# Performance work log

Measured on AMD Instinct MI355X. Metric: run time of the kernel, lower is better.

Reference implementation:

```python
import jax, jax.numpy as jnp
import numpy as np

N_NODES = 10000
N_EDGES = 640000
IN_CH = 128
HID = 256
OUT_CH = 10
NUM_GRAPHS = 64
EPS = 0.0  # non-trainable buffer, initial_eps=0


def setup_inputs() -> dict:
    key = jax.random.key(0)
    ks = jax.random.split(key, 12)
    x = jax.random.normal(ks[0], (N_NODES, IN_CH), dtype=jnp.float32)
    edge_index = jax.random.randint(ks[1], (2, N_EDGES), 0, N_NODES, dtype=jnp.int64)
    batch = jnp.sort(jax.random.randint(ks[2], (N_NODES,), 0, NUM_GRAPHS, dtype=jnp.int64))
    edge_weights = jax.random.uniform(ks[3], (N_EDGES,), dtype=jnp.float32)
    def lin(k, fan_in, fan_out):
        bound = 1.0 / np.sqrt(fan_in)
        kw, kb = jax.random.split(k)
        W = jax.random.uniform(kw, (fan_out, fan_in), minval=-bound, maxval=bound, dtype=jnp.float32)
        b = jax.random.uniform(kb, (fan_out,), minval=-bound, maxval=bound, dtype=jnp.float32)
        return W, b
    W1, b1 = lin(ks[4], IN_CH, HID)
    W2, b2 = lin(ks[5], HID, HID)
    W3, b3 = lin(ks[6], HID, HID)
    Wl, bl = lin(ks[7], HID, OUT_CH)
    return {"x": x, "edge_index": edge_index, "batch": batch, "edge_weights": edge_weights,
            "W1": W1, "b1": b1, "W2": W2, "b2": b2, "W3": W3, "b3": b3, "Wl": Wl, "bl": bl}


def _ginw_conv(x, edge_index, edge_weights, W, b):
    # message: edge_weight * x_j (source nodes), aggregated by add at target i
    src, dst = edge_index[0], edge_index[1]
    msg = edge_weights[:, None] * x[src]           # [E, F]
    agg = jax.ops.segment_sum(msg, dst, num_segments=N_NODES)  # [N, F]
    out = agg + (1.0 + EPS) * x
    return out @ W.T + b


def reference(x, edge_index, batch, edge_weights, W1, b1, W2, b2, W3, b3, Wl, bl):
    h = jax.nn.relu(_ginw_conv(x, edge_index, edge_weights, W1, b1))
    h = jax.nn.relu(_ginw_conv(h, edge_index, edge_weights, W2, b2))
    h = jax.nn.relu(_ginw_conv(h, edge_index, edge_weights, W3, b3))
    # global mean pool over graphs
    sums = jax.ops.segment_sum(h, batch, num_segments=NUM_GRAPHS)        # [G, HID]
    cnts = jax.ops.segment_sum(jnp.ones((N_NODES,), h.dtype), batch, num_segments=NUM_GRAPHS)
    pooled = sums / jnp.maximum(cnts, 1.0)[:, None]
    return pooled @ Wl.T + bl
```

## Files before the change

### kernel.cpp

```cpp
#include <hip/hip_runtime.h>
#include <hip/hip_fp16.h>

namespace {
constexpr int NN   = 10000;
constexpr int NE   = 640000;
constexpr int INC  = 128;
constexpr int HIDC = 256;
constexpr int OUTC = 10;
constexpr int NG   = 64;
constexpr int PP   = 8;

constexpr int NB     = 157;
constexpr int G1     = 256;
constexpr int CHUNK1 = NE / G1;
constexpr int CAPB   = 64;
constexpr int LCAP   = 5120;
}

typedef __attribute__((ext_vector_type(8))) short short8;
typedef __attribute__((ext_vector_type(4))) float f32x4;

__device__ __forceinline__ ushort f2bf(float f) {
    uint u = __float_as_uint(f);
    uint r = u + 0x7FFFu + ((u >> 16) & 1u);
    return (ushort)(r >> 16);
}
__device__ __forceinline__ float bf2f(ushort u) {
    return __uint_as_float(((uint)u) << 16);
}
__device__ __forceinline__ float rec_w(uint rec) {
    return __half2float(__ushort_as_half((ushort)(rec & 0xFFFFu)));
}

__global__ __launch_bounds__(256) void partition_kernel(const int* __restrict__ ei,
                                                        const float* __restrict__ ew,
                                                        uint2* __restrict__ stag,
                                                        int* __restrict__ cnts,
                                                        int* __restrict__ cnts_T,
                                                        const float* __restrict__ x,
                                                        ushort* __restrict__ xb,
                                                        const float* __restrict__ W1,
                                                        ushort* __restrict__ w1b,
                                                        const float* __restrict__ W2,
                                                        ushort* __restrict__ w2b,
                                                        const float* __restrict__ W3,
                                                        ushort* __restrict__ w3b) {
    __shared__ int lcnt[NB];
    const int t = threadIdx.x, g = blockIdx.x;
    for (int i = t; i < NB; i += 256) lcnt[i] = 0;
    __syncthreads();
    const int base = g * CHUNK1;
    for (int i = t; i < CHUNK1; i += 256) {
        const int e = base + i;
        const int dst = ei[NE + e];
        const int src = ei[e];
        const ushort hw = __half_as_ushort(__float2half(ew[e]));
        const int bk = dst >> 6;
        const int idx = atomicAdd(&lcnt[bk], 1);
        if (idx < CAPB)
            stag[((size_t)g * NB + bk) * CAPB + idx] =
                make_uint2(((uint)src << 16) | (uint)hw, (uint)dst);
    }
    __syncthreads();
    for (int i = t; i < NB; i += 256) {
        const int c = min(lcnt[i], CAPB);
        cnts[g * NB + i] = c;
        cnts_T[i * G1 + g] = c;
    }
    const int gt = g * 256 + t, gs = G1 * 256;
    {
        const int n4 = NN * INC / 4;
        for (int i = gt; i < n4; i += gs) {
            float4 v = ((const float4*)x)[i];
            ushort4 o; o.x = f2bf(v.x); o.y = f2bf(v.y); o.z = f2bf(v.z); o.w = f2bf(v.w);
            ((ushort4*)xb)[i] = o;
        }
    }
    {
        const int n4 = HIDC * INC / 4;
        for (int i = gt; i < n4; i += gs) {
            float4 v = ((const float4*)W1)[i];
            ushort4 o; o.x = f2bf(v.x); o.y = f2bf(v.y); o.z = f2bf(v.z); o.w = f2bf(v.w);
            ((ushort4*)w1b)[i] = o;
        }
    }
    {
        const int n4 = HIDC * HIDC / 4;
        for (int i = gt; i < n4; i += gs) {
            float4 v = ((const float4*)W2)[i];
            ushort4 o; o.x = f2bf(v.x); o.y = f2bf(v.y); o.z = f2bf(v.z); o.w = f2bf(v.w);
            ((ushort4*)w2b)[i] = o;
            float4 v3 = ((const float4*)W3)[i];
            ushort4 o3; o3.x = f2bf(v3.x); o3.y = f2bf(v3.y); o3.z = f2bf(v3.z); o3.w = f2bf(v3.w);
            ((ushort4*)w3b)[i] = o3;
        }
    }
}

__global__ __launch_bounds__(1024) void place_kernel(const uint2* __restrict__ stag,
                                                     const int* __restrict__ cnts,
                                                     const int* __restrict__ cnts_T,
                                                     int* __restrict__ row_start,
                                                     uint* __restrict__ erec) {
    const int b = blockIdx.x;
    const int t = threadIdx.x;
    __shared__ int part[256];
    __shared__ int foff[G1 + 1];
    __shared__ int h[64];
    __shared__ int curl[64];
    __shared__ uint2 srec[LCAP];

    {
        int s = 0;
        if (t < NB) {
            const int4* r = (const int4*)(cnts_T + (size_t)t * G1);
#pragma unroll 8
            for (int i = 0; i < G1 / 4; i++) {
                int4 v = r[i];
                s += v.x + v.y + v.z + v.w;
            }
        }
        if (t < 256) part[t] = s;
        __syncthreads();
        for (int off = 1; off < 256; off <<= 1) {
            int v = 0;
            if (t < 256 && t >= off) v = part[t - off];
            __syncthreads();
            if (t < 256) part[t] += v;
            __syncthreads();
        }
    }
    const int bs = (b == 0) ? 0 : part[b - 1];
    if (b == 0 && t == 0) row_start[NN] = part[NB - 1];
    __syncthreads();

    {
        int c = 0;
        if (t < 256) c = cnts[t * NB + b];
        if (t < 256) part[t] = c;
        if (t < 64) h[t] = 0;
        __syncthreads();
        for (int off = 1; off < 256; off <<= 1) {
            int v = 0;
            if (t < 256 && t >= off) v = part[t - off];
            __syncthreads();
            if (t < 256) part[t] += v;
            __syncthreads();
        }
        if (t < 256) foff[t] = part[t] - c;
        if (t == 0) foff[G1] = part[255];
        __syncthreads();
    }
    const int Rb = foff[G1];

    for (int r = t; r < Rb; r += 1024) {
        int lo = 0, hi = G1;
        while (hi - lo > 1) { int mid = (lo + hi) >> 1; if (foff[mid] <= r) lo = mid; else hi = mid; }
        uint2 rec = stag[((size_t)lo * NB + b) * CAPB + (r - foff[lo])];
        if (r < LCAP) srec[r] = rec;
        atomicAdd(&h[rec.y & 63], 1);
    }
    __syncthreads();

    {
        const int hv = (t < 64) ? h[t] : 0;
        if (t < 256) part[t] = (t < 64) ? hv : 0;
        __syncthreads();
        for (int off = 1; off < 64; off <<= 1) {
            int v = 0;
            if (t < 256 && t >= off) v = part[t - off];
            __syncthreads();
            if (t < 256) part[t] += v;
            __syncthreads();
        }
        if (t < 64) {
            const int excl = part[t] - hv;
            const int node = b * 64 + t;
            if (node < NN) row_start[node] = bs + excl;
            curl[t] = excl;
        }
        __syncthreads();
    }

    for (int r = t; r < Rb; r += 1024) {
        uint2 rec;
        if (r < LCAP) rec = srec[r];
        else {
            int lo = 0, hi = G1;
            while (hi - lo > 1) { int mid = (lo + hi) >> 1; if (foff[mid] <= r) lo = mid; else hi = mid; }
            rec = stag[((size_t)lo * NB + b) * CAPB + (r - foff[lo])];
        }
        const int pos = bs + atomicAdd(&curl[rec.y & 63], 1);
        erec[pos] = rec.x;
    }
}

template <int F>
__global__ __launch_bounds__(256) void gather_bf16_kernel(const int* __restrict__ row_start,
                                                          const uint* __restrict__ erec,
                                                          const ushort* __restrict__ x,
                                                          ushort* __restrict__ out) {
    constexpr int VEC = F / 64;
    constexpr int U = 12;
    const int n = blockIdx.x * 4 + (threadIdx.x >> 6);
    const int lane = threadIdx.x & 63;
    if (n >= NN) return;
    const int beg = row_start[n];
    const int end = row_start[n + 1];
    const size_t loff = (size_t)lane * VEC;

    float acc[VEC];
    {
        ushort v[VEC];
        if (VEC == 4) *(ushort4*)v = *(const ushort4*)(x + (size_t)n * F + loff);
        else          *(ushort2*)v = *(const ushort2*)(x + (size_t)n * F + loff);
#pragma unroll
        for (int i = 0; i < VEC; i++) acc[i] = bf2f(v[i]);
    }

    int e = beg;
    for (; e + U <= end; e += U) {
        uint rec[U];
#pragma unroll
        for (int u = 0; u < U; u++) rec[u] = erec[e + u];
        ushort v[U][VEC];
#pragma unroll
        for (int u = 0; u < U; u++) {
            const ushort* r = x + (size_t)(rec[u] >> 16) * F + loff;
            if (VEC == 4) *(ushort4*)v[u] = *(const ushort4*)r;
            else          *(ushort2*)v[u] = *(const ushort2*)r;
        }
#pragma unroll
        for (int u = 0; u < U; u++) {
            const float w = rec_w(rec[u]);
#pragma unroll
            for (int i = 0; i < VEC; i++) acc[i] += w * bf2f(v[u][i]);
        }
    }
    for (; e < end; e++) {
        uint rec = erec[e];
        const float w = rec_w(rec);
        ushort v[VEC];
        const ushort* r = x + (size_t)(rec >> 16) * F + loff;
        if (VEC == 4) *(ushort4*)v = *(const ushort4*)r;
        else          *(ushort2*)v = *(const ushort2*)r;
#pragma unroll
        for (int i = 0; i < VEC; i++) acc[i] += w * bf2f(v[i]);
    }

    ushort o[VEC];
#pragma unroll
    for (int i = 0; i < VEC; i++) o[i] = f2bf(acc[i]);
    if (VEC == 4) *(ushort4*)(out + (size_t)n * F + loff) = *(ushort4*)o;
    else          *(ushort2*)(out + (size_t)n * F + loff) = *(ushort2*)o;
}

__global__ __launch_bounds__(256) void gather_bf16_half_kernel(const int* __restrict__ row_start,
                                                               const uint* __restrict__ erec,
                                                               const ushort* __restrict__ x,
                                                               ushort* __restrict__ out) {
    constexpr int U = 16;
    const int half = blockIdx.x & 1;
    const int n = (blockIdx.x >> 1) * 4 + (threadIdx.x >> 6);
    const int lane = threadIdx.x & 63;
    if (n >= NN) return;
    const int beg = row_start[n];
    const int end = row_start[n + 1];
    const size_t loff = (size_t)half * 128 + lane * 2;

    float acc0, acc1;
    {
        ushort2 v = *(const ushort2*)(x + (size_t)n * HIDC + loff);
        acc0 = bf2f(v.x);
        acc1 = bf2f(v.y);
    }

    int e = beg;
    for (; e + U <= end; e += U) {
        uint rec[U];
#pragma unroll
        for (int u = 0; u < U; u++) rec[u] = erec[e + u];
        ushort2 v[U];
#pragma unroll
        for (int u = 0; u < U; u++)
            v[u] = *(const ushort2*)(x + (size_t)(rec[u] >> 16) * HIDC + loff);
#pragma unroll
        for (int u = 0; u < U; u++) {
            const float w = rec_w(rec[u]);
            acc0 += w * bf2f(v[u].x);
            acc1 += w * bf2f(v[u].y);
        }
    }
    for (; e < end; e++) {
        uint rec = erec[e];
        const float w = rec_w(rec);
        ushort2 v = *(const ushort2*)(x + (size_t)(rec >> 16) * HIDC + loff);
        acc0 += w * bf2f(v.x);
        acc1 += w * bf2f(v.y);
    }

    ushort2 o;
    o.x = f2bf(acc0);
    o.y = f2bf(acc1);
    *(ushort2*)(out + (size_t)n * HIDC + loff) = o;
}

template <int K>
__global__ __launch_bounds__(256) void mfma_gemm_kernel(const ushort* __restrict__ A,
                                                        const ushort* __restrict__ Wb,
                                                        const float* __restrict__ bias,
                                                        ushort* __restrict__ C, int M) {
    constexpr int LDW = K + 8;
    __shared__ ushort Ws[64 * LDW];
    const int tid = threadIdx.x;
    const int bm = blockIdx.x * 128;
    const int bn = blockIdx.y * 64;

    constexpr int CPR = K / 8;
    for (int idx = tid; idx < 64 * CPR; idx += 256) {
        int r = idx / CPR, c = idx % CPR;
        uint4 v = *(const uint4*)(Wb + (size_t)(bn + r) * K + c * 8);
        *(uint4*)(&Ws[r * LDW + c * 8]) = v;
    }
    __syncthreads();

    const int wave = tid >> 6;
    const int lane = tid & 63;
    const int lrow = lane & 15;
    const int lq   = lane >> 4;
    const int m0 = bm + wave * 32;

    f32x4 acc[2][4] = {};
    const int r0 = min(m0 + lrow, M - 1);
    const int r1 = min(m0 + 16 + lrow, M - 1);

    for (int k0 = 0; k0 < K; k0 += 32) {
        const int kk = k0 + lq * 8;
        short8 a0 = *(const short8*)(A + (size_t)r0 * K + kk);
        short8 a1 = *(const short8*)(A + (size_t)r1 * K + kk);
        short8 b[4];
#pragma unroll
        for (int j = 0; j < 4; j++)
            b[j] = *(const short8*)(&Ws[(j * 16 + lrow) * LDW + kk]);
#pragma unroll
        for (int j = 0; j < 4; j++) {
            acc[0][j] = __builtin_amdgcn_mfma_f32_16x16x32_bf16(a0, b[j], acc[0][j], 0, 0, 0);
            acc[1][j] = __builtin_amdgcn_mfma_f32_16x16x32_bf16(a1, b[j], acc[1][j], 0, 0, 0);
        }
    }

#pragma unroll
    for (int sub = 0; sub < 2; sub++) {
#pragma unroll
        for (int j = 0; j < 4; j++) {
            const int gn = bn + j * 16 + lrow;
            const float bv = bias[gn];
#pragma unroll
            for (int i = 0; i < 4; i++) {
                const int gm = m0 + sub * 16 + lq * 4 + i;
                if (gm < M) {
                    float v = acc[sub][j][i] + bv;
                    v = fmaxf(v, 0.0f);
                    C[(size_t)gm * HIDC + gn] = f2bf(v);
                }
            }
        }
    }
}

__device__ __forceinline__ int lower_bound_batch(const int* __restrict__ batch, int val) {
    int lo = 0, hi = NN;
    while (lo < hi) {
        int mid = (lo + hi) >> 1;
        if (batch[mid] < val) lo = mid + 1;
        else hi = mid;
    }
    return lo;
}

__global__ __launch_bounds__(256) void pool_partial_kernel(const ushort* __restrict__ h,
                                                           const int* __restrict__ batch,
                                                           float* __restrict__ partials) {
    const int g = blockIdx.x;
    const int p = blockIdx.y;
    const int c = threadIdx.x;
    const int lo = lower_bound_batch(batch, g);
    const int hi = lower_bound_batch(batch, g + 1);
    const int cnt = hi - lo;
    const int chunk = (cnt + PP - 1) / PP;
    const int n0 = lo + p * chunk;
    const int n1 = min(hi, n0 + chunk);
    float sum = 0.0f;
    for (int n = n0; n < n1; n++) sum += bf2f(h[(size_t)n * HIDC + c]);
    partials[((size_t)g * PP + p) * HIDC + c] = sum;
}

__global__ __launch_bounds__(256) void head_kernel(const float* __restrict__ partials,
                                                   const int* __restrict__ batch,
                                                   const float* __restrict__ Wl,
                                                   const float* __restrict__ bl,
                                                   float* __restrict__ out) {
    __shared__ float s[HIDC];
    const int g = blockIdx.x;
    const int c = threadIdx.x;
    const int lo = lower_bound_batch(batch, g);
    const int hi = lower_bound_batch(batch, g + 1);
    const float inv = 1.0f / fmaxf((float)(hi - lo), 1.0f);
    float sum = 0.0f;
#pragma unroll
    for (int p = 0; p < PP; p++) sum += partials[((size_t)g * PP + p) * HIDC + c];
    s[c] = sum * inv;
    __syncthreads();
    if (c < OUTC) {
        float acc = bl[c];
        for (int k = 0; k < HIDC; k++) acc += s[k] * Wl[(size_t)c * HIDC + k];
        out[(size_t)g * OUTC + c] = acc;
    }
}

extern "C" void kernel_launch(void* const* d_in, const int* in_sizes, int n_in,
                              void* d_out, int out_size, void* d_ws, size_t ws_size,
                              hipStream_t stream) {
    const float* x     = (const float*)d_in[0];
    const int*   ei    = (const int*)d_in[1];
    const int*   batch = (const int*)d_in[2];
    const float* ew    = (const float*)d_in[3];
    const float* W1    = (const float*)d_in[4];
    const float* b1    = (const float*)d_in[5];
    const float* W2    = (const float*)d_in[6];
    const float* b2    = (const float*)d_in[7];
    const float* W3    = (const float*)d_in[8];
    const float* b3    = (const float*)d_in[9];
    const float* Wl    = (const float*)d_in[10];
    const float* bl    = (const float*)d_in[11];

    char* p = (char*)d_ws;
    uint2*  stag   = (uint2*)p;  p += (size_t)G1 * NB * CAPB * 8;
    ushort* xb     = (ushort*)p; p += (size_t)NN * INC * 2;
    ushort* agg128 = (ushort*)p; p += (size_t)NN * INC * 2;
    ushort* agg256 = (ushort*)p; p += (size_t)NN * HIDC * 2;
    ushort* h      = (ushort*)p; p += (size_t)NN * HIDC * 2;
    ushort* w1b    = (ushort*)p; p += (size_t)HIDC * INC * 2;
    ushort* w2b    = (ushort*)p; p += (size_t)HIDC * HIDC * 2;
    ushort* w3b    = (ushort*)p; p += (size_t)HIDC * HIDC * 2;
    uint*   erec   = (uint*)p;   p += (size_t)NE * 4;
    float*  partials = (float*)p; p += (size_t)NG * PP * HIDC * 4;
    int*    cnts   = (int*)p;    p += (size_t)G1 * NB * 4;
    int*    cnts_T = (int*)p;    p += (size_t)NB * G1 * 4;
    int*    row_start = (int*)p; p += 40016;

    partition_kernel<<<G1, 256, 0, stream>>>(ei, ew, stag, cnts, cnts_T, x, xb,
                                             W1, w1b, W2, w2b, W3, w3b);
    place_kernel<<<NB, 1024, 0, stream>>>(stag, cnts, cnts_T, row_start, erec);

    const int gather_grid = (NN + 3) / 4;
    dim3 gemm_grid((NN + 127) / 128, HIDC / 64);

    gather_bf16_kernel<INC><<<gather_grid, 256, 0, stream>>>(row_start, erec, xb, agg128);
    mfma_gemm_kernel<INC><<<gemm_grid, 256, 0, stream>>>(agg128, w1b, b1, h, NN);

    gather_bf16_half_kernel<<<gather_grid * 2, 256, 0, stream>>>(row_start, erec, h, agg256);
    mfma_gemm_kernel<HIDC><<<gemm_grid, 256, 0, stream>>>(agg256, w2b, b2, h, NN);

    gather_bf16_half_kernel<<<gather_grid * 2, 256, 0, stream>>>(row_start, erec, h, agg256);
    mfma_gemm_kernel<HIDC><<<gemm_grid, 256, 0, stream>>>(agg256, w3b, b3, h, NN);

    pool_partial_kernel<<<dim3(NG, PP), 256, 0, stream>>>(h, batch, partials);
    head_kernel<<<NG, 256, 0, stream>>>(partials, batch, Wl, bl, (float*)d_out);
}
```

Before: 237.8 us.

## Switch bf16 pipeline to fp16 with packed half FMA gathers and fused pool-head

Activations and weights are now stored as fp16 instead of bf16. The gathers accumulate with packed half2 FMAs in two fp16 accumulators instead of converting to fp32, and the GEMMs use the f16 MFMA. Loads and stores are marked nontemporal, staging records become packed 64-bit words, and the pool and head kernels merge into one launch. Accumulating in fp16 over roughly 64 neighbors cuts ALU work but risks precision loss or overflow in the aggregated sums.

```diff
diff --git a/kernel.cpp b/kernel.cpp
--- a/kernel.cpp
+++ b/kernel.cpp
@@ -8,7 +8,6 @@
 constexpr int HIDC = 256;
 constexpr int OUTC = 10;
 constexpr int NG   = 64;
-constexpr int PP   = 8;
 
 constexpr int NB     = 157;
 constexpr int G1     = 256;
@@ -17,34 +16,31 @@
 constexpr int LCAP   = 5120;
 }
 
-typedef __attribute__((ext_vector_type(8))) short short8;
+typedef __attribute__((ext_vector_type(8))) _Float16 half8;
+typedef __attribute__((ext_vector_type(2))) _Float16 h16x2;
 typedef __attribute__((ext_vector_type(4))) float f32x4;
-
-__device__ __forceinline__ ushort f2bf(float f) {
-    uint u = __float_as_uint(f);
-    uint r = u + 0x7FFFu + ((u >> 16) & 1u);
-    return (ushort)(r >> 16);
-}
-__device__ __forceinline__ float bf2f(ushort u) {
-    return __uint_as_float(((uint)u) << 16);
-}
-__device__ __forceinline__ float rec_w(uint rec) {
-    return __half2float(__ushort_as_half((ushort)(rec & 0xFFFFu)));
+typedef __attribute__((ext_vector_type(4))) ushort u16x4;
+typedef unsigned long long u64;
+
+__device__ __forceinline__ ushort f2h(float f) { return __half_as_ushort(__float2half(f)); }
+__device__ __forceinline__ float h2f(ushort u) { return __half2float(__ushort_as_half(u)); }
+__device__ __forceinline__ _Float16 bits2h(ushort u) {
+    union { ushort u; _Float16 h; } c; c.u = u; return c.h;
 }
 
 __global__ __launch_bounds__(256) void partition_kernel(const int* __restrict__ ei,
                                                         const float* __restrict__ ew,
-                                                        uint2* __restrict__ stag,
+                                                        u64* __restrict__ stag,
                                                         int* __restrict__ cnts,
                                                         int* __restrict__ cnts_T,
                                                         const float* __restrict__ x,
-                                                        ushort* __restrict__ xb,
+                                                        ushort* __restrict__ xh,
                                                         const float* __restrict__ W1,
-                                                        ushort* __restrict__ w1b,
+                                                        ushort* __restrict__ w1h,
                                                         const float* __restrict__ W2,
-                                                        ushort* __restrict__ w2b,
+                                                        ushort* __restrict__ w2h,
                                                         const float* __restrict__ W3,
-                                                        ushort* __restrict__ w3b) {
+                                                        ushort* __restrict__ w3h) {
     __shared__ int lcnt[NB];
     const int t = threadIdx.x, g = blockIdx.x;
     for (int i = t; i < NB; i += 256) lcnt[i] = 0;
@@ -52,14 +48,14 @@
     const int base = g * CHUNK1;
     for (int i = t; i < CHUNK1; i += 256) {
         const int e = base + i;
-        const int dst = ei[NE + e];
-        const int src = ei[e];
-        const ushort hw = __half_as_ushort(__float2half(ew[e]));
+        const int dst = __builtin_nontemporal_load(ei + NE + e);
+        const int src = __builtin_nontemporal_load(ei + e);
+        const ushort hw = __half_as_ushort(__float2half(__builtin_nontemporal_load(ew + e)));
         const int bk = dst >> 6;
         const int idx = atomicAdd(&lcnt[bk], 1);
         if (idx < CAPB)
             stag[((size_t)g * NB + bk) * CAPB + idx] =
-                make_uint2(((uint)src << 16) | (uint)hw, (uint)dst);
+                ((u64)(uint)dst << 32) | ((uint)src << 16) | (uint)hw;
     }
     __syncthreads();
     for (int i = t; i < NB; i += 256) {
@@ -71,33 +67,41 @@
     {
         const int n4 = NN * INC / 4;
         for (int i = gt; i < n4; i += gs) {
-            float4 v = ((const float4*)x)[i];
-            ushort4 o; o.x = f2bf(v.x); o.y = f2bf(v.y); o.z = f2bf(v.z); o.w = f2bf(v.w);
-            ((ushort4*)xb)[i] = o;
+            f32x4 v = __builtin_nontemporal_load((const f32x4*)x + i);
+            u16x4 o;
+#pragma unroll
+            for (int j = 0; j < 4; j++) o[j] = f2h(v[j]);
+            __builtin_nontemporal_store(o, (u16x4*)xh + i);
         }
     }
     {
         const int n4 = HIDC * INC / 4;
         for (int i = gt; i < n4; i += gs) {
-            float4 v = ((const float4*)W1)[i];
-            ushort4 o; o.x = f2bf(v.x); o.y = f2bf(v.y); o.z = f2bf(v.z); o.w = f2bf(v.w);
-            ((ushort4*)w1b)[i] = o;
+            f32x4 v = __builtin_nontemporal_load((const f32x4*)W1 + i);
+            u16x4 o;
+#pragma unroll
+            for (int j = 0; j < 4; j++) o[j] = f2h(v[j]);
+            __builtin_nontemporal_store(o, (u16x4*)w1h + i);
         }
     }
     {
         const int n4 = HIDC * HIDC / 4;
         for (int i = gt; i < n4; i += gs) {
-            float4 v = ((const float4*)W2)[i];
-            ushort4 o; o.x = f2bf(v.x); o.y = f2bf(v.y); o.z = f2bf(v.z); o.w = f2bf(v.w);
-            ((ushort4*)w2b)[i] = o;
-            float4 v3 = ((const float4*)W3)[i];
-            ushort4 o3; o3.x = f2bf(v3.x); o3.y = f2bf(v3.y); o3.z = f2bf(v3.z); o3.w = f2bf(v3.w);
-            ((ushort4*)w3b)[i] = o3;
-        }
-    }
-}
-
-__global__ __launch_bounds__(1024) void place_kernel(const uint2* __restrict__ stag,
+            f32x4 v = __builtin_nontemporal_load((const f32x4*)W2 + i);
+            u16x4 o;
+#pragma unroll
+            for (int j = 0; j < 4; j++) o[j] = f2h(v[j]);
+            __builtin_nontemporal_store(o, (u16x4*)w2h + i);
+            f32x4 v3 = __builtin_nontemporal_load((const f32x4*)W3 + i);
+            u16x4 o3;
+#pragma unroll
+            for (int j = 0; j < 4; j++) o3[j] = f2h(v3[j]);
+            __builtin_nontemporal_store(o3, (u16x4*)w3h + i);
+        }
+    }
+}
+
+__global__ __launch_bounds__(1024) void place_kernel(const u64* __restrict__ stag,
                                                      const int* __restrict__ cnts,
                                                      const int* __restrict__ cnts_T,
                                                      int* __restrict__ row_start,
@@ -108,7 +112,7 @@
     __shared__ int foff[G1 + 1];
     __shared__ int h[64];
     __shared__ int curl[64];
-    __shared__ uint2 srec[LCAP];
+    __shared__ u64 srec[LCAP];
 
     {
         int s = 0;
@@ -156,9 +160,9 @@
     for (int r = t; r < Rb; r += 1024) {
         int lo = 0, hi = G1;
         while (hi - lo > 1) { int mid = (lo + hi) >> 1; if (foff[mid] <= r) lo = mid; else hi = mid; }
-        uint2 rec = stag[((size_t)lo * NB + b) * CAPB + (r - foff[lo])];
+        u64 rec = __builtin_nontemporal_load(&stag[((size_t)lo * NB + b) * CAPB + (r - foff[lo])]);
         if (r < LCAP) srec[r] = rec;
-        atomicAdd(&h[rec.y & 63], 1);
+        atomicAdd(&h[(uint)(rec >> 32) & 63], 1);
     }
     __syncthreads();
 
@@ -183,82 +187,69 @@
     }
 
     for (int r = t; r < Rb; r += 1024) {
-        uint2 rec;
+        u64 rec;
         if (r < LCAP) rec = srec[r];
         else {
             int lo = 0, hi = G1;
             while (hi - lo > 1) { int mid = (lo + hi) >> 1; if (foff[mid] <= r) lo = mid; else hi = mid; }
-            rec = stag[((size_t)lo * NB + b) * CAPB + (r - foff[lo])];
-        }
-        const int pos = bs + atomicAdd(&curl[rec.y & 63], 1);
-        erec[pos] = rec.x;
-    }
-}
-
-template <int F>
-__global__ __launch_bounds__(256) void gather_bf16_kernel(const int* __restrict__ row_start,
-                                                          const uint* __restrict__ erec,
-                                                          const ushort* __restrict__ x,
-                                                          ushort* __restrict__ out) {
-    constexpr int VEC = F / 64;
-    constexpr int U = 12;
+            rec = __builtin_nontemporal_load(&stag[((size_t)lo * NB + b) * CAPB + (r - foff[lo])]);
+        }
+        const int pos = bs + atomicAdd(&curl[(uint)(rec >> 32) & 63], 1);
+        erec[pos] = (uint)rec;
+    }
+}
+
+__global__ __launch_bounds__(256) void gather128_kernel(const int* __restrict__ row_start,
+                                                        const uint* __restrict__ erec,
+                                                        const ushort* __restrict__ x,
+                                                        ushort* __restrict__ out) {
+    constexpr int U = 16;
     const int n = blockIdx.x * 4 + (threadIdx.x >> 6);
     const int lane = threadIdx.x & 63;
     if (n >= NN) return;
     const int beg = row_start[n];
     const int end = row_start[n + 1];
-    const size_t loff = (size_t)lane * VEC;
-
-    float acc[VEC];
-    {
-        ushort v[VEC];
-        if (VEC == 4) *(ushort4*)v = *(const ushort4*)(x + (size_t)n * F + loff);
-        else          *(ushort2*)v = *(const ushort2*)(x + (size_t)n * F + loff);
-#pragma unroll
-        for (int i = 0; i < VEC; i++) acc[i] = bf2f(v[i]);
-    }
+    const size_t loff = (size_t)lane * 2;
+    const ushort* xr = x + loff;
+
+    h16x2 aa = *(const h16x2*)(x + (size_t)n * INC + loff);
+    h16x2 ab = {(_Float16)0.f, (_Float16)0.f};
 
     int e = beg;
     for (; e + U <= end; e += U) {
         uint rec[U];
 #pragma unroll
         for (int u = 0; u < U; u++) rec[u] = erec[e + u];
-        ushort v[U][VEC];
+        h16x2 v[U];
+#pragma unroll
+        for (int u = 0; u < U; u++)
+            v[u] = *(const h16x2*)(xr + (size_t)(rec[u] >> 16) * INC);
 #pragma unroll
         for (int u = 0; u < U; u++) {
-            const ushort* r = x + (size_t)(rec[u] >> 16) * F + loff;
-            if (VEC == 4) *(ushort4*)v[u] = *(const ushort4*)r;
-            else          *(ushort2*)v[u] = *(const ushort2*)r;
-        }
-#pragma unroll
-        for (int u = 0; u < U; u++) {
-            const float w = rec_w(rec[u]);
-#pragma unroll
-            for (int i = 0; i < VEC; i++) acc[i] += w * bf2f(v[u][i]);
+            const _Float16 wh = bits2h((ushort)(rec[u] & 0xFFFFu));
+            const h16x2 w2 = {wh, wh};
+            if (u & 1) ab = v[u] * w2 + ab;
+            else       aa = v[u] * w2 + aa;
         }
     }
     for (; e < end; e++) {
-        uint rec = erec[e];
-        const float w = rec_w(rec);
-        ushort v[VEC];
-        const ushort* r = x + (size_t)(rec >> 16) * F + loff;
-        if (VEC == 4) *(ushort4*)v = *(const ushort4*)r;
-        else          *(ushort2*)v = *(const ushort2*)r;
-#pragma unroll
-        for (int i = 0; i < VEC; i++) acc[i] += w * bf2f(v[i]);
-    }
-
-    ushort o[VEC];
-#pragma unroll
-    for (int i = 0; i < VEC; i++) o[i] = f2bf(acc[i]);
-    if (VEC == 4) *(ushort4*)(out + (size_t)n * F + loff) = *(ushort4*)o;
-    else          *(ushort2*)(out + (size_t)n * F + loff) = *(ushort2*)o;
-}
-
-__global__ __launch_bounds__(256) void gather_bf16_half_kernel(const int* __restrict__ row_start,
-                                                               const uint* __restrict__ erec,
-                                                               const ushort* __restrict__ x,
-                                                               ushort* __restrict__ out) {
+        const uint rec = erec[e];
+        const _Float16 wh = bits2h((ushort)(rec & 0xFFFFu));
+        const h16x2 w2 = {wh, wh};
+        const h16x2 v = *(const h16x2*)(xr + (size_t)(rec >> 16) * INC);
+        aa = v * w2 + aa;
+    }
+
+    h16x2 o = aa + ab;
+    uint ob;
+    __builtin_memcpy(&ob, &o, 4);
+    __builtin_nontemporal_store(ob, (uint*)(out + (size_t)n * INC + loff));
+}
+
+__global__ __launch_bounds__(256) void gather_half_kernel(const int* __restrict__ row_start,
+                                                          const uint* __restrict__ erec,
+                                                          const ushort* __restrict__ x,
+                                                          ushort* __restrict__ out) {
     constexpr int U = 16;
     const int half = blockIdx.x & 1;
     const int n = (blockIdx.x >> 1) * 4 + (threadIdx.x >> 6);
@@ -267,42 +258,40 @@
     const int beg = row_start[n];
     const int end = row_start[n + 1];
     const size_t loff = (size_t)half * 128 + lane * 2;
-
-    float acc0, acc1;
-    {
-        ushort2 v = *(const ushort2*)(x + (size_t)n * HIDC + loff);
-        acc0 = bf2f(v.x);
-        acc1 = bf2f(v.y);
-    }
+    const ushort* xr = x + loff;
+
+    h16x2 aa = *(const h16x2*)(x + (size_t)n * HIDC + loff);
+    h16x2 ab = {(_Float16)0.f, (_Float16)0.f};
 
     int e = beg;
     for (; e + U <= end; e += U) {
         uint rec[U];
 #pragma unroll
         for (int u = 0; u < U; u++) rec[u] = erec[e + u];
-        ushort2 v[U];
+        h16x2 v[U];
 #pragma unroll
         for (int u = 0; u < U; u++)
-            v[u] = *(const ushort2*)(x + (size_t)(rec[u] >> 16) * HIDC + loff);
+            v[u] = *(const h16x2*)(xr + (size_t)(rec[u] >> 16) * HIDC);
 #pragma unroll
         for (int u = 0; u < U; u++) {
-            const float w = rec_w(rec[u]);
-            acc0 += w * bf2f(v[u].x);
-            acc1 += w * bf2f(v[u].y);
+            const _Float16 wh = bits2h((ushort)(rec[u] & 0xFFFFu));
+            const h16x2 w2 = {wh, wh};
+            if (u & 1) ab = v[u] * w2 + ab;
+            else       aa = v[u] * w2 + aa;
         }
     }
     for (; e < end; e++) {
-        uint rec = erec[e];
-        const float w = rec_w(rec);
-        ushort2 v = *(const ushort2*)(x + (size_t)(rec >> 16) * HIDC + loff);
-        acc0 += w * bf2f(v.x);
-        acc1 += w * bf2f(v.y);
-    }
-
-    ushort2 o;
-    o.x = f2bf(acc0);
-    o.y = f2bf(acc1);
-    *(ushort2*)(out + (size_t)n * HIDC + loff) = o;
+        const uint rec = erec[e];
+        const _Float16 wh = bits2h((ushort)(rec & 0xFFFFu));
+        const h16x2 w2 = {wh, wh};
+        const h16x2 v = *(const h16x2*)(xr + (size_t)(rec >> 16) * HIDC);
+        aa = v * w2 + aa;
+    }
+
+    h16x2 o = aa + ab;
+    uint ob;
+    __builtin_memcpy(&ob, &o, 4);
+    __builtin_nontemporal_store(ob, (uint*)(out + (size_t)n * HIDC + loff));
 }
 
 template <int K>
@@ -336,16 +325,16 @@
 
     for (int k0 = 0; k0 < K; k0 += 32) {
         const int kk = k0 + lq * 8;
-        short8 a0 = *(const short8*)(A + (size_t)r0 * K + kk);
-        short8 a1 = *(const short8*)(A + (size_t)r1 * K + kk);
-        short8 b[4];
+        half8 a0 = __builtin_nontemporal_load((const half8*)(A + (size_t)r0 * K + kk));
+        half8 a1 = __builtin_nontemporal_load((const half8*)(A + (size_t)r1 * K + kk));
+        half8 b[4];
 #pragma unroll
         for (int j = 0; j < 4; j++)
-            b[j] = *(const short8*)(&Ws[(j * 16 + lrow) * LDW + kk]);
+            b[j] = *(const half8*)(&Ws[(j * 16 + lrow) * LDW + kk]);
 #pragma unroll
         for (int j = 0; j < 4; j++) {
-            acc[0][j] = __builtin_amdgcn_mfma_f32_16x16x32_bf16(a0, b[j], acc[0][j], 0, 0, 0);
-            acc[1][j] = __builtin_amdgcn_mfma_f32_16x16x32_bf16(a1, b[j], acc[1][j], 0, 0, 0);
+            acc[0][j] = __builtin_amdgcn_mfma_f32_16x16x32_f16(a0, b[j], acc[0][j], 0, 0, 0);
+            acc[1][j] = __builtin_amdgcn_mfma_f32_16x16x32_f16(a1, b[j], acc[1][j], 0, 0, 0);
         }
     }
 
@@ -361,7 +350,7 @@
                 if (gm < M) {
                     float v = acc[sub][j][i] + bv;
                     v = fmaxf(v, 0.0f);
-                    C[(size_t)gm * HIDC + gn] = f2bf(v);
+                    C[(size_t)gm * HIDC + gn] = f2h(v);
                 }
             }
         }
@@ -378,43 +367,50 @@
     return lo;
 }
 
-__global__ __launch_bounds__(256) void pool_partial_kernel(const ushort* __restrict__ h,
-                                                           const int* __restrict__ batch,
-                                                           float* __restrict__ partials) {
+__global__ __launch_bounds__(512) void pool_head_kernel(const ushort* __restrict__ h,
+                                                        const int* __restrict__ batch,
+                                                        const float* __restrict__ Wl,
+                                                        const float* __restrict__ bl,
+                                                        float* __restrict__ out) {
+    __shared__ float s[8][HIDC];
+    __shared__ float s2[OUTC][8];
     const int g = blockIdx.x;
-    const int p = blockIdx.y;
-    const int c = threadIdx.x;
+    const int t = threadIdx.x;
+    const int p = t >> 6;
+    const int c0 = (t & 63) * 4;
     const int lo = lower_bound_batch(batch, g);
     const int hi = lower_bound_batch(batch, g + 1);
-    const int cnt = hi - lo;
-    const int chunk = (cnt + PP - 1) / PP;
-    const int n0 = lo + p * chunk;
-    const int n1 = min(hi, n0 + chunk);
-    float sum = 0.0f;
-    for (int n = n0; n < n1; n++) sum += bf2f(h[(size_t)n * HIDC + c]);
-    partials[((size_t)g * PP + p) * HIDC + c] = sum;
-}
-
-__global__ __launch_bounds__(256) void head_kernel(const float* __restrict__ partials,
-                                                   const int* __restrict__ batch,
-                                                   const float* __restrict__ Wl,
-                                                   const float* __restrict__ bl,
-                                                   float* __restrict__ out) {
-    __shared__ float s[HIDC];
-    const int g = blockIdx.x;
-    const int c = threadIdx.x;
-    const int lo = lower_bound_batch(batch, g);
-    const int hi = lower_bound_batch(batch, g + 1);
-    const float inv = 1.0f / fmaxf((float)(hi - lo), 1.0f);
-    float sum = 0.0f;
-#pragma unroll
-    for (int p = 0; p < PP; p++) sum += partials[((size_t)g * PP + p) * HIDC + c];
-    s[c] = sum * inv;
-    __syncthreads();
-    if (c < OUTC) {
-        float acc = bl[c];
-        for (int k = 0; k < HIDC; k++) acc += s[k] * Wl[(size_t)c * HIDC + k];
-        out[(size_t)g * OUTC + c] = acc;
+
+    float a0 = 0.f, a1 = 0.f, a2 = 0.f, a3 = 0.f;
+    for (int n = lo + p; n < hi; n += 8) {
+        u16x4 v = *(const u16x4*)(h + (size_t)n * HIDC + c0);
+        a0 += h2f(v[0]); a1 += h2f(v[1]); a2 += h2f(v[2]); a3 += h2f(v[3]);
+    }
+    s[p][c0 + 0] = a0; s[p][c0 + 1] = a1; s[p][c0 + 2] = a2; s[p][c0 + 3] = a3;
+    __syncthreads();
+
+    if (t < HIDC) {
+        const float inv = 1.0f / fmaxf((float)(hi - lo), 1.0f);
+        float m = 0.f;
+#pragma unroll
+        for (int q = 0; q < 8; q++) m += s[q][t];
+        s[0][t] = m * inv;
+    }
+    __syncthreads();
+
+    if (t < OUTC * 8) {
+        const int oc = t >> 3, q = t & 7;
+        float acc = 0.f;
+        for (int k = q * 32; k < q * 32 + 32; k++)
+            acc += s[0][k] * Wl[(size_t)oc * HIDC + k];
+        s2[oc][q] = acc;
+    }
+    __syncthreads();
+    if (t < OUTC) {
+        float acc = bl[t];
+#pragma unroll
+        for (int q = 0; q < 8; q++) acc += s2[t][q];
+        out[(size_t)g * OUTC + t] = acc;
     }
 }
 
@@ -435,36 +431,34 @@
     const float* bl    = (const float*)d_in[11];
 
     char* p = (char*)d_ws;
-    uint2*  stag   = (uint2*)p;  p += (size_t)G1 * NB * CAPB * 8;
-    ushort* xb     = (ushort*)p; p += (size_t)NN * INC * 2;
+    u64*    stag   = (u64*)p;    p += (size_t)G1 * NB * CAPB * 8;
+    ushort* xh     = (ushort*)p; p += (size_t)NN * INC * 2;
     ushort* agg128 = (ushort*)p; p += (size_t)NN * INC * 2;
     ushort* agg256 = (ushort*)p; p += (size_t)NN * HIDC * 2;
     ushort* h      = (ushort*)p; p += (size_t)NN * HIDC * 2;
-    ushort* w1b    = (ushort*)p; p += (size_t)HIDC * INC * 2;
-    ushort* w2b    = (ushort*)p; p += (size_t)HIDC * HIDC * 2;
-    ushort* w3b    = (ushort*)p; p += (size_t)HIDC * HIDC * 2;
+    ushort* w1h    = (ushort*)p; p += (size_t)HIDC * INC * 2;
+    ushort* w2h    = (ushort*)p; p += (size_t)HIDC * HIDC * 2;
+    ushort* w3h    = (ushort*)p; p += (size_t)HIDC * HIDC * 2;
     uint*   erec   = (uint*)p;   p += (size_t)NE * 4;
-    float*  partials = (float*)p; p += (size_t)NG * PP * HIDC * 4;
     int*    cnts   = (int*)p;    p += (size_t)G1 * NB * 4;
     int*    cnts_T = (int*)p;    p += (size_t)NB * G1 * 4;
     int*    row_start = (int*)p; p += 40016;
 
-    partition_kernel<<<G1, 256, 0, stream>>>(ei, ew, stag, cnts, cnts_T, x, xb,
-                                             W1, w1b, W2, w2b, W3, w3b);
+    partition_kernel<<<G1, 256, 0, stream>>>(ei, ew, stag, cnts, cnts_T, x, xh,
+                                             W1, w1h, W2, w2h, W3, w3h);
     place_kernel<<<NB, 1024, 0, stream>>>(stag, cnts, cnts_T, row_start, erec);
 
     const int gather_grid = (NN + 3) / 4;
     dim3 gemm_grid((NN + 127) / 128, HIDC / 64);
 
-    gather_bf16_kernel<INC><<<gather_grid, 256, 0, stream>>>(row_start, erec, xb, agg128);
-    mfma_gemm_kernel<INC><<<gemm_grid, 256, 0, stream>>>(agg128, w1b, b1, h, NN);
-
-    gather_bf16_half_kernel<<<gather_grid * 2, 256, 0, stream>>>(row_start, erec, h, agg256);
-    mfma_gemm_kernel<HIDC><<<gemm_grid, 256, 0, stream>>>(agg256, w2b, b2, h, NN);
-
-    gather_bf16_half_kernel<<<gather_grid * 2, 256, 0, stream>>>(row_start, erec, h, agg256);
-    mfma_gemm_kernel<HIDC><<<gemm_grid, 256, 0, stream>>>(agg256, w3b, b3, h, NN);
-
-    pool_partial_kernel<<<dim3(NG, PP), 256, 0, stream>>>(h, batch, partials);
-    head_kernel<<<NG, 256, 0, stream>>>(partials, batch, Wl, bl, (float*)d_out);
-}
+    gather128_kernel<<<gather_grid, 256, 0, stream>>>(row_start, erec, xh, agg128);
+    mfma_gemm_kernel<INC><<<gemm_grid, 256, 0, stream>>>(agg128, w1h, b1, h, NN);
+
+    gather_half_kernel<<<gather_grid * 2, 256, 0, stream>>>(row_start, erec, h, agg256);
+    mfma_gemm_kernel<HIDC><<<gemm_grid, 256, 0, stream>>>(agg256, w2h, b2, h, NN);
+
+    gather_half_kernel<<<gather_grid * 2, 256, 0, stream>>>(row_start, erec, h, agg256);
+    mfma_gemm_kernel<HIDC><<<gemm_grid, 256, 0, stream>>>(agg256, w3h, b3, h, NN);
+
+    pool_head_kernel<<<NG, 512, 0, stream>>>(h, batch, Wl, bl, (float*)d_out);
+}
```

New measurement: 240.3 us. About the same (+1.1%).
